# Performance work log

Measured on AMD Instinct MI355X. Metric: run time of the kernel, lower is better.

## Reference

```python
import jax, jax.numpy as jnp
import numpy as np

B, C, H, W = 32, 1024, 32, 32  # NOTE: code requires C == H*W (see bmm below)
C_HALF = C // 2


def setup_inputs() -> dict:
    key = jax.random.key(0)
    ks = jax.random.split(key, 7)
    s_in = 1.0 / np.sqrt(C)
    return {
        "x": jax.random.normal(ks[0], (B, C, H, W), dtype=jnp.float32),
        "Wq": jax.random.normal(ks[1], (C_HALF, C), dtype=jnp.float32) * s_in,
        "bq": jax.random.normal(ks[2], (C_HALF,), dtype=jnp.float32) * 0.01,
        "Wk": jax.random.normal(ks[3], (C_HALF, C), dtype=jnp.float32) * s_in,
        "bk": jax.random.normal(ks[4], (C_HALF,), dtype=jnp.float32) * 0.01,
        "Wv": jax.random.normal(ks[5], (C, C), dtype=jnp.float32) * s_in,
        "bv": jax.random.normal(ks[6], (C,), dtype=jnp.float32) * 0.01,
    }


def reference(x, Wq, bq, Wk, bk, Wv, bv):
    b, c, h, w = x.shape
    hw = h * w
    xf = x.reshape(b, c, hw)  # [B, C, HW]
    # 1x1 convs are per-pixel linear maps over channels
    q = jnp.einsum('oc,bcn->bno', Wq, xf) + bq            # [B, HW, C/2]  (permuted)
    k = jnp.einsum('oc,bcn->bon', Wk, xf) + bk[:, None]   # [B, C/2, HW]
    v = jnp.einsum('oc,bcn->bno', Wv, xf) + bv            # [B, HW, C]   (permuted)
    attn = jax.nn.softmax(jnp.einsum('bno,bom->bnm', q, k), axis=-1)  # [B, HW, HW]
    # torch: bmm(value [B,HW,C], attention^T [B,HW,HW]) -> requires C == HW
    out = jnp.einsum('bik,bjk->bij', v, attn)  # [B, HW(=C), HW]
    out = out.reshape(b, c, h, w)
    return out + x
```

## Files before the change

kernel.cpp:

```cpp
#include <hip/hip_runtime.h>

typedef _Float16 f16;
typedef _Float16 f16x8 __attribute__((ext_vector_type(8)));
typedef float f32x16 __attribute__((ext_vector_type(16)));

__device__ __forceinline__ void g2lds16(const void* g, void* l) {
    __builtin_amdgcn_global_load_lds(
        (const __attribute__((address_space(1))) void*)g,
        (__attribute__((address_space(3))) void*)l, 16, 0, 0);
}

__global__ __launch_bounds__(256)
void prep_w(const float* __restrict__ Wq, const float* __restrict__ bq,
            const float* __restrict__ Wk, const float* __restrict__ bk,
            const float* __restrict__ Wv, const float* __restrict__ bv,
            f16* __restrict__ Wall, float* __restrict__ ball)
{
    const int idx = blockIdx.x * 256 + threadIdx.x;
    const int o = idx >> 10;
    const int c = idx & 1023;
    float w;
    if (o < 512)        w = Wq[idx];
    else if (o < 1024)  w = Wk[idx - 512 * 1024];
    else                w = Wv[idx - 1024 * 1024];
    Wall[idx] = (f16)w;
    if (c == 0)
        ball[o] = (o < 512) ? bq[o] : (o < 1024) ? bk[o - 512] : bv[o - 1024];
}

__global__ __launch_bounds__(256)
void transpose_cast(const float* __restrict__ x, f16* __restrict__ xT)
{
    __shared__ float t[64][65];
    const int b  = blockIdx.z;
    const int c0 = blockIdx.y << 6;
    const int n0 = blockIdx.x << 6;
    const int tid = threadIdx.x;
    const float* xb = x + (unsigned long long)b * (1024ull * 1024ull);

    {
        const int cl = tid >> 4;
        const int n4 = (tid & 15) << 2;
#pragma unroll
        for (int i = 0; i < 64; i += 16) {
            const float4 v = *(const float4*)(xb + (unsigned long long)(c0 + cl + i) * 1024ull + (n0 + n4));
            t[cl + i][n4 + 0] = v.x; t[cl + i][n4 + 1] = v.y;
            t[cl + i][n4 + 2] = v.z; t[cl + i][n4 + 3] = v.w;
        }
    }
    __syncthreads();
    {
        f16* ob = xT + (unsigned long long)b * (1024ull * 1024ull);
        const int nl = tid >> 3;
        const int c8 = (tid & 7) << 3;
#pragma unroll
        for (int i = 0; i < 64; i += 32) {
            f16x8 h;
#pragma unroll
            for (int j = 0; j < 8; ++j) h[j] = (f16)t[c8 + j][nl + i];
            *(f16x8*)(ob + (unsigned long long)(n0 + nl + i) * 1024ull + (c0 + c8)) = h;
        }
    }
}

template <int EPI, int LDA, int LDB, int K, int LDO,
          long long SA, long long SB, long long SO, int SWZ>
__global__ __launch_bounds__(256, 4)
void gemm_nt(const f16* __restrict__ A, const f16* __restrict__ Bm,
             const float* __restrict__ bias,
             f16* __restrict__ Oh, float* __restrict__ Of,
             const float* __restrict__ Xres)
{
    __shared__ f16 As[128 * 64];
    __shared__ f16 Bs[128 * 64];

    const int tid  = threadIdx.x;
    const int wave = tid >> 6;
    const int lane = tid & 63;
    const int l31  = lane & 31;
    const int half = lane >> 5;
    const int wr   = (wave >> 1) << 6;
    const int wc   = (wave & 1) << 6;

    int bm, bn, bz = blockIdx.z;
    if (SWZ == 1) {
        const int xcd   = blockIdx.x & 7;
        const int local = blockIdx.x >> 3;
        const int stl   = local >> 5;
        const int sub   = local & 31;
        const int bng   = xcd & 1;
        const int g4    = stl * 4 + (xcd >> 1);
        bm = (g4 * 4 + (sub & 3)) << 7;
        bn = (bng * 8 + (sub >> 2)) << 7;
    } else if (SWZ == 2) {
        const int xcd   = blockIdx.x & 7;
        const int local = blockIdx.x >> 3;
        const int unit  = local >> 5;
        const int wi    = local & 31;
        const int pp    = unit * 8 + xcd;
        bz = pp >> 1;
        const int bh = pp & 1;
        bm = (wi & 7) << 7;
        bn = ((bh << 2) + (wi >> 3)) << 7;
    } else {
        bm = blockIdx.x << 7;
        bn = blockIdx.y << 7;
    }

    const f16* Ab = A  + (unsigned long long)bz * (unsigned long long)SA;
    const f16* Bb = Bm + (unsigned long long)bz * (unsigned long long)SB;

    const int srow = lane >> 3;
    const int scol = (((lane & 7) ^ srow) << 3);

    f32x16 acc[2][2] = {};

    for (int k0 = 0; k0 < K; k0 += 64) {
        __syncthreads();
#pragma unroll
        for (int t = 0; t < 4; ++t) {
            const int rb = t * 32 + wave * 8;
            g2lds16(Ab + (unsigned long long)(bm + rb + srow) * LDA + (k0 + scol),
                    As + rb * 64 + lane * 8);
            g2lds16(Bb + (unsigned long long)(bn + rb + srow) * LDB + (k0 + scol),
                    Bs + rb * 64 + lane * 8);
        }
        __syncthreads();

#pragma unroll
        for (int ks = 0; ks < 4; ++ks) {
            const int kg = ks * 2 + half;
            f16x8 af[2], bf[2];
#pragma unroll
            for (int i = 0; i < 2; ++i) {
                const int ra = wr + i * 32 + l31;
                af[i] = *(const f16x8*)(As + ra * 64 + ((kg ^ (ra & 7)) << 3));
                const int rbn = wc + i * 32 + l31;
                bf[i] = *(const f16x8*)(Bs + rbn * 64 + ((kg ^ (rbn & 7)) << 3));
            }
#pragma unroll
            for (int mi = 0; mi < 2; ++mi)
#pragma unroll
                for (int ni = 0; ni < 2; ++ni)
                    acc[mi][ni] = __builtin_amdgcn_mfma_f32_32x32x16_f16(
                        af[mi], bf[ni], acc[mi][ni], 0, 0, 0);
        }
    }

#pragma unroll
    for (int mi = 0; mi < 2; ++mi) {
#pragma unroll
        for (int ni = 0; ni < 2; ++ni) {
            const int col = bn + wc + ni * 32 + l31;
            float bc = 0.0f;
            if (EPI == 0) bc = bias[col];
#pragma unroll
            for (int r = 0; r < 16; ++r) {
                const int row = bm + wr + mi * 32 + (r & 3) + 8 * (r >> 2) + 4 * half;
                const float val = acc[mi][ni][r];
                if (EPI == 0) {
                    Oh[(unsigned long long)row * LDO + col] = (f16)(val + bc);
                } else if (EPI == 1) {
                    Of[(unsigned long long)bz * (unsigned long long)SO +
                       (unsigned long long)row * LDO + col] = val;
                } else {
                    const unsigned long long off =
                        (unsigned long long)bz * (unsigned long long)SO +
                        (unsigned long long)row * LDO + col;
                    Of[off] = val + Xres[off];
                }
            }
        }
    }
}

__global__ __launch_bounds__(512)
void qk_softmax(const f16* __restrict__ QKV, f16* __restrict__ P)
{
    __shared__ f16 Qs[32 * 512];
    __shared__ f16 Ks[512 * 64];
    __shared__ float redm[8][2][16];
    __shared__ float reds[8][2][16];

    const int tid  = threadIdx.x;
    const int wave = tid >> 6;
    const int lane = tid & 63;
    const int l31  = lane & 31;
    const int half = lane >> 5;

    const int xcd   = blockIdx.x & 7;
    const int local = blockIdx.x >> 3;
    const int batch = xcd * 4 + (local >> 5);
    const int jt    = local & 31;
    const int j0    = jt << 5;

    const f16* Qb = QKV + (unsigned long long)batch * (1024ull * 2048ull);
    const f16* Kb = Qb + 512;

#pragma unroll
    for (int i = 0; i < 4; ++i) {
        const int row = wave * 4 + i;
        g2lds16(Qb + (unsigned long long)(j0 + row) * 2048ull + ((lane ^ (row & 7)) << 3),
                Qs + row * 512 + lane * 8);
    }

    f32x16 acc[4] = {};
    const int wkey = wave << 7;

    for (int d0 = 0; d0 < 512; d0 += 32) {
        __syncthreads();
#pragma unroll
        for (int t = 0; t < 8; ++t) {
            const int rb  = wave * 64 + t * 8;
            const int R   = rb + (lane >> 3);
            const int p   = (lane & 7) ^ (R & 7);
            const int key = (R << 1) + (p >> 2);
            const int slt = p & 3;
            g2lds16(Kb + (unsigned long long)key * 2048ull + d0 + (slt << 3),
                    Ks + rb * 64 + lane * 8);
        }
        __syncthreads();
#pragma unroll
        for (int ks = 0; ks < 2; ++ks) {
            const int sl = ks * 2 + half;
            const int gs = (d0 >> 3) + sl;
            const f16x8 af = *(const f16x8*)(Qs + l31 * 512 + ((gs ^ (l31 & 7)) << 3));
#pragma unroll
            for (int ni = 0; ni < 4; ++ni) {
                const int key = wkey + ni * 32 + l31;
                const int R   = key >> 1;
                const int p   = ((key & 1) << 2) + sl;
                const f16x8 bf = *(const f16x8*)(Ks + R * 64 + ((p ^ (R & 7)) << 3));
                acc[ni] = __builtin_amdgcn_mfma_f32_32x32x16_f16(af, bf, acc[ni], 0, 0, 0);
            }
        }
    }

    float mx[16];
#pragma unroll
    for (int r = 0; r < 16; ++r) {
        float m = fmaxf(fmaxf(acc[0][r], acc[1][r]), fmaxf(acc[2][r], acc[3][r]));
#pragma unroll
        for (int off = 16; off; off >>= 1)
            m = fmaxf(m, __shfl_xor(m, off, 64));
        mx[r] = m;
    }
    if (l31 == 0) {
#pragma unroll
        for (int r = 0; r < 16; ++r) redm[wave][half][r] = mx[r];
    }
    __syncthreads();
#pragma unroll
    for (int r = 0; r < 16; ++r) {
        float m = redm[0][half][r];
#pragma unroll
        for (int w = 1; w < 8; ++w) m = fmaxf(m, redm[w][half][r]);
        mx[r] = m;
    }

    float sm[16];
#pragma unroll
    for (int r = 0; r < 16; ++r) sm[r] = 0.0f;
#pragma unroll
    for (int ni = 0; ni < 4; ++ni)
#pragma unroll
        for (int r = 0; r < 16; ++r) {
            const float e = __expf(acc[ni][r] - mx[r]);
            acc[ni][r] = e;
            sm[r] += e;
        }
#pragma unroll
    for (int r = 0; r < 16; ++r) {
#pragma unroll
        for (int off = 16; off; off >>= 1)
            sm[r] += __shfl_xor(sm[r], off, 64);
    }
    if (l31 == 0) {
#pragma unroll
        for (int r = 0; r < 16; ++r) reds[wave][half][r] = sm[r];
    }
    __syncthreads();
#pragma unroll
    for (int r = 0; r < 16; ++r) {
        float s = reds[0][half][r];
#pragma unroll
        for (int w = 1; w < 8; ++w) s += reds[w][half][r];
        sm[r] = 1.0f / s;
    }

    f16* Pt = Ks;
#pragma unroll
    for (int ni = 0; ni < 4; ++ni)
#pragma unroll
        for (int r = 0; r < 16; ++r) {
            const int row = (r & 3) + 8 * (r >> 2) + 4 * half;
            const int key = wkey + ni * 32 + l31;
            Pt[row * 1024 + key] = (f16)(acc[ni][r] * sm[r]);
        }
    __syncthreads();

    f16* Pg = P + ((unsigned long long)batch * 1024ull + j0) * 1024ull;
#pragma unroll
    for (int i = 0; i < 8; ++i)
        *(f16x8*)(Pg + i * 4096 + tid * 8) = *(const f16x8*)(Pt + i * 4096 + tid * 8);
}

extern "C" void kernel_launch(void* const* d_in, const int* in_sizes, int n_in,
                              void* d_out, int out_size, void* d_ws, size_t ws_size,
                              hipStream_t stream)
{
    const float* x  = (const float*)d_in[0];
    const float* Wq = (const float*)d_in[1];
    const float* bq = (const float*)d_in[2];
    const float* Wk = (const float*)d_in[3];
    const float* bk = (const float*)d_in[4];
    const float* Wv = (const float*)d_in[5];
    const float* bv = (const float*)d_in[6];
    float* out = (float*)d_out;

    f16*   xT   = (f16*)d_ws;
    f16*   Wall = xT + 32ull * 1024 * 1024;
    float* ball = (float*)(Wall + 2048ull * 1024);
    f16*   QKV  = (f16*)(ball + 2048);
    f16*   P    = QKV + 64ull * 1024 * 1024;

    prep_w<<<8192, 256, 0, stream>>>(Wq, bq, Wk, bk, Wv, bv, Wall, ball);
    transpose_cast<<<dim3(16, 16, 32), 256, 0, stream>>>(x, xT);

    gemm_nt<0, 1024, 1024, 1024, 2048, 0ll, 0ll, 0ll, 1>
        <<<dim3(4096, 1, 1), 256, 0, stream>>>(
        xT, Wall, ball, QKV, nullptr, nullptr);

    qk_softmax<<<dim3(1024, 1, 1), 512, 0, stream>>>(QKV, P);

    gemm_nt<2, 2048, 1024, 1024, 1024, 1024ll * 2048, 1024ll * 1024, 1024ll * 1024, 2>
        <<<dim3(2048, 1, 1), 256, 0, stream>>>(
        QKV + 1024, P, nullptr, nullptr, out, x);
}
```

Before: 650.4 us.

## Double query tile per block and double-buffer per-wave K loads in qk_softmax

The QK^T+softmax kernel now processes 64 query rows per block instead of 32, halving the grid and reusing each loaded K tile for twice as many rows. K loads become per-wave, double-buffered direct-to-LDS transfers gated by vmcnt waits instead of block-wide syncthreads, and MFMA sections get raised scheduling priority. This is meant to cut K reload traffic and barrier stalls, at the cost of more LDS (~96KB) and doubled accumulator registers, which may reduce occupancy. The softmax reductions and P write-out are done in two passes.

Measured after the change: 600.2 us. 1.08x faster.

```diff
diff --git a/kernel.cpp b/kernel.cpp
--- a/kernel.cpp
+++ b/kernel.cpp
@@ -177,10 +177,10 @@
 __global__ __launch_bounds__(512)
 void qk_softmax(const f16* __restrict__ QKV, f16* __restrict__ P)
 {
-    __shared__ f16 Qs[32 * 512];
-    __shared__ f16 Ks[512 * 64];
-    __shared__ float redm[8][2][16];
-    __shared__ float reds[8][2][16];
+    __shared__ f16 Qs[64 * 512];
+    __shared__ f16 Ks[2 * 8 * 2048];
+    __shared__ float redm[8][2][2][16];
+    __shared__ float reds[8][2][2][16];
 
     const int tid  = threadIdx.x;
     const int wave = tid >> 6;
@@ -190,119 +190,159 @@
 
     const int xcd   = blockIdx.x & 7;
     const int local = blockIdx.x >> 3;
-    const int batch = xcd * 4 + (local >> 5);
-    const int jt    = local & 31;
-    const int j0    = jt << 5;
+    const int batch = xcd * 4 + (local >> 4);
+    const int j0    = (local & 15) << 6;
 
     const f16* Qb = QKV + (unsigned long long)batch * (1024ull * 2048ull);
     const f16* Kb = Qb + 512;
 
 #pragma unroll
-    for (int i = 0; i < 4; ++i) {
-        const int row = wave * 4 + i;
-        g2lds16(Qb + (unsigned long long)(j0 + row) * 2048ull + ((lane ^ (row & 7)) << 3),
+    for (int i = 0; i < 8; ++i) {
+        const int row = wave * 8 + i;
+        g2lds16(Qb + (unsigned long long)(j0 + row) * 2048ull + ((lane ^ i) << 3),
                 Qs + row * 512 + lane * 8);
     }
-
-    f32x16 acc[4] = {};
-    const int wkey = wave << 7;
-
-    for (int d0 = 0; d0 < 512; d0 += 32) {
+    const int lu = lane ^ ((lane >> 3) & 1);
+    const f16* Kw = Kb + (unsigned long long)(wave * 128 + (lu >> 1)) * 2048ull
+                       + ((lu & 1) << 3);
+    f16* KsW = Ks + wave * 2048;
+#pragma unroll
+    for (int i = 0; i < 4; ++i)
+        g2lds16(Kw + i * (32 * 2048), KsW + i * 512 + lane * 8);
+
+    asm volatile("s_waitcnt vmcnt(0)" ::: "memory");
+    __builtin_amdgcn_sched_barrier(0);
+    __syncthreads();
+
+    const int r7 = l31 & 7;
+    const int sb = ((l31 << 1) + half) ^ ((l31 >> 2) & 1);
+    const f16* KsR = Ks + wave * 2048 + sb * 8;
+
+    f32x16 acc[2][4] = {};
+
+    for (int tt = 0; tt < 16; ++tt) {
+#pragma unroll
+        for (int p = 0; p < 2; ++p) {
+            const int t = tt * 2 + p;
+            if (t < 31) {
+#pragma unroll
+                for (int i = 0; i < 4; ++i)
+                    g2lds16(Kw + (t + 1) * 16 + i * (32 * 2048),
+                            KsW + (p ^ 1) * 16384 + i * 512 + lane * 8);
+                asm volatile("s_waitcnt vmcnt(4)" ::: "memory");
+            } else {
+                asm volatile("s_waitcnt vmcnt(0)" ::: "memory");
+            }
+            __builtin_amdgcn_sched_barrier(0);
+
+            const int gs = t * 2 + half;
+            f16x8 af[2];
+#pragma unroll
+            for (int sub = 0; sub < 2; ++sub)
+                af[sub] = *(const f16x8*)(Qs + (sub * 32 + l31) * 512 + ((gs ^ r7) << 3));
+            f16x8 bf[4];
+#pragma unroll
+            for (int ni = 0; ni < 4; ++ni)
+                bf[ni] = *(const f16x8*)(KsR + p * 16384 + ni * 512);
+
+            __builtin_amdgcn_s_setprio(1);
+#pragma unroll
+            for (int sub = 0; sub < 2; ++sub)
+#pragma unroll
+                for (int ni = 0; ni < 4; ++ni)
+                    acc[sub][ni] = __builtin_amdgcn_mfma_f32_32x32x16_f16(
+                        af[sub], bf[ni], acc[sub][ni], 0, 0, 0);
+            __builtin_amdgcn_s_setprio(0);
+        }
+    }
+
+    float mx[2][16];
+#pragma unroll
+    for (int sub = 0; sub < 2; ++sub)
+#pragma unroll
+        for (int r = 0; r < 16; ++r) {
+            float m = fmaxf(fmaxf(acc[sub][0][r], acc[sub][1][r]),
+                            fmaxf(acc[sub][2][r], acc[sub][3][r]));
+#pragma unroll
+            for (int off = 16; off; off >>= 1)
+                m = fmaxf(m, __shfl_xor(m, off, 64));
+            mx[sub][r] = m;
+        }
+    if (l31 == 0) {
+#pragma unroll
+        for (int sub = 0; sub < 2; ++sub)
+#pragma unroll
+            for (int r = 0; r < 16; ++r) redm[wave][sub][half][r] = mx[sub][r];
+    }
+    __syncthreads();
+#pragma unroll
+    for (int sub = 0; sub < 2; ++sub)
+#pragma unroll
+        for (int r = 0; r < 16; ++r) {
+            float m = redm[0][sub][half][r];
+#pragma unroll
+            for (int w = 1; w < 8; ++w) m = fmaxf(m, redm[w][sub][half][r]);
+            mx[sub][r] = m;
+        }
+
+    float sm[2][16];
+#pragma unroll
+    for (int sub = 0; sub < 2; ++sub)
+#pragma unroll
+        for (int r = 0; r < 16; ++r) sm[sub][r] = 0.0f;
+#pragma unroll
+    for (int sub = 0; sub < 2; ++sub)
+#pragma unroll
+        for (int ni = 0; ni < 4; ++ni)
+#pragma unroll
+            for (int r = 0; r < 16; ++r) {
+                const float e = __expf(acc[sub][ni][r] - mx[sub][r]);
+                acc[sub][ni][r] = e;
+                sm[sub][r] += e;
+            }
+#pragma unroll
+    for (int sub = 0; sub < 2; ++sub)
+#pragma unroll
+        for (int r = 0; r < 16; ++r) {
+#pragma unroll
+            for (int off = 16; off; off >>= 1)
+                sm[sub][r] += __shfl_xor(sm[sub][r], off, 64);
+        }
+    if (l31 == 0) {
+#pragma unroll
+        for (int sub = 0; sub < 2; ++sub)
+#pragma unroll
+            for (int r = 0; r < 16; ++r) reds[wave][sub][half][r] = sm[sub][r];
+    }
+    __syncthreads();
+#pragma unroll
+    for (int sub = 0; sub < 2; ++sub)
+#pragma unroll
+        for (int r = 0; r < 16; ++r) {
+            float s = reds[0][sub][half][r];
+#pragma unroll
+            for (int w = 1; w < 8; ++w) s += reds[w][sub][half][r];
+            sm[sub][r] = 1.0f / s;
+        }
+
+    f16* Pt = Ks;
+#pragma unroll
+    for (int pass = 0; pass < 2; ++pass) {
         __syncthreads();
 #pragma unroll
-        for (int t = 0; t < 8; ++t) {
-            const int rb  = wave * 64 + t * 8;
-            const int R   = rb + (lane >> 3);
-            const int p   = (lane & 7) ^ (R & 7);
-            const int key = (R << 1) + (p >> 2);
-            const int slt = p & 3;
-            g2lds16(Kb + (unsigned long long)key * 2048ull + d0 + (slt << 3),
-                    Ks + rb * 64 + lane * 8);
-        }
+        for (int ni = 0; ni < 4; ++ni)
+#pragma unroll
+            for (int r = 0; r < 16; ++r) {
+                const int row = (r & 3) + 8 * (r >> 2) + 4 * half;
+                const int key = (wave << 7) + ni * 32 + l31;
+                Pt[row * 1024 + key] = (f16)(acc[pass][ni][r] * sm[pass][r]);
+            }
         __syncthreads();
-#pragma unroll
-        for (int ks = 0; ks < 2; ++ks) {
-            const int sl = ks * 2 + half;
-            const int gs = (d0 >> 3) + sl;
-            const f16x8 af = *(const f16x8*)(Qs + l31 * 512 + ((gs ^ (l31 & 7)) << 3));
-#pragma unroll
-            for (int ni = 0; ni < 4; ++ni) {
-                const int key = wkey + ni * 32 + l31;
-                const int R   = key >> 1;
-                const int p   = ((key & 1) << 2) + sl;
-                const f16x8 bf = *(const f16x8*)(Ks + R * 64 + ((p ^ (R & 7)) << 3));
-                acc[ni] = __builtin_amdgcn_mfma_f32_32x32x16_f16(af, bf, acc[ni], 0, 0, 0);
-            }
-        }
-    }
-
-    float mx[16];
-#pragma unroll
-    for (int r = 0; r < 16; ++r) {
-        float m = fmaxf(fmaxf(acc[0][r], acc[1][r]), fmaxf(acc[2][r], acc[3][r]));
-#pragma unroll
-        for (int off = 16; off; off >>= 1)
-            m = fmaxf(m, __shfl_xor(m, off, 64));
-        mx[r] = m;
-    }
-    if (l31 == 0) {
-#pragma unroll
-        for (int r = 0; r < 16; ++r) redm[wave][half][r] = mx[r];
-    }
-    __syncthreads();
-#pragma unroll
-    for (int r = 0; r < 16; ++r) {
-        float m = redm[0][half][r];
-#pragma unroll
-        for (int w = 1; w < 8; ++w) m = fmaxf(m, redm[w][half][r]);
-        mx[r] = m;
-    }
-
-    float sm[16];
-#pragma unroll
-    for (int r = 0; r < 16; ++r) sm[r] = 0.0f;
-#pragma unroll
-    for (int ni = 0; ni < 4; ++ni)
-#pragma unroll
-        for (int r = 0; r < 16; ++r) {
-            const float e = __expf(acc[ni][r] - mx[r]);
-            acc[ni][r] = e;
-            sm[r] += e;
-        }
-#pragma unroll
-    for (int r = 0; r < 16; ++r) {
-#pragma unroll
-        for (int off = 16; off; off >>= 1)
-            sm[r] += __shfl_xor(sm[r], off, 64);
-    }
-    if (l31 == 0) {
-#pragma unroll
-        for (int r = 0; r < 16; ++r) reds[wave][half][r] = sm[r];
-    }
-    __syncthreads();
-#pragma unroll
-    for (int r = 0; r < 16; ++r) {
-        float s = reds[0][half][r];
-#pragma unroll
-        for (int w = 1; w < 8; ++w) s += reds[w][half][r];
-        sm[r] = 1.0f / s;
-    }
-
-    f16* Pt = Ks;
-#pragma unroll
-    for (int ni = 0; ni < 4; ++ni)
-#pragma unroll
-        for (int r = 0; r < 16; ++r) {
-            const int row = (r & 3) + 8 * (r >> 2) + 4 * half;
-            const int key = wkey + ni * 32 + l31;
-            Pt[row * 1024 + key] = (f16)(acc[ni][r] * sm[r]);
-        }
-    __syncthreads();
-
-    f16* Pg = P + ((unsigned long long)batch * 1024ull + j0) * 1024ull;
-#pragma unroll
-    for (int i = 0; i < 8; ++i)
-        *(f16x8*)(Pg + i * 4096 + tid * 8) = *(const f16x8*)(Pt + i * 4096 + tid * 8);
+        f16* Pg = P + ((unsigned long long)batch * 1024ull + j0 + pass * 32) * 1024ull;
+#pragma unroll
+        for (int i = 0; i < 8; ++i)
+            *(f16x8*)(Pg + i * 4096 + tid * 8) = *(const f16x8*)(Pt + i * 4096 + tid * 8);
+    }
 }
 
 extern "C" void kernel_launch(void* const* d_in, const int* in_sizes, int n_in,
@@ -331,7 +371,7 @@
         <<<dim3(4096, 1, 1), 256, 0, stream>>>(
         xT, Wall, ball, QKV, nullptr, nullptr);
 
-    qk_softmax<<<dim3(1024, 1, 1), 512, 0, stream>>>(QKV, P);
+    qk_softmax<<<dim3(512, 1, 1), 512, 0, stream>>>(QKV, P);
 
     gemm_nt<2, 2048, 1024, 1024, 1024, 1024ll * 2048, 1024ll * 1024, 1024ll * 1024, 2>
         <<<dim3(2048, 1, 1), 256, 0, stream>>>(
```

## Load Q/K fragments directly from global into registers in qk_softmax

Applied to the files above, without the earlier changes.

Replaces the LDS-staged Q and K tiles (global_load_lds plus two barriers per k-step) with direct per-lane global vector loads into MFMA operand registers, double-buffered two steps ahead. LDS is cut to just the P output staging buffer, and launch bounds now request 4 blocks per CU for higher occupancy. This removes the per-iteration barriers and LDS traffic. In exchange, each wave reads K rows straight from global/L2 with strided 16-byte accesses, with no sharing of Q across waves through LDS, which may raise cache traffic.

Measured after the change: 666.2 us. 1.02x slower.

```diff
diff --git a/kernel.cpp b/kernel.cpp
--- a/kernel.cpp
+++ b/kernel.cpp
@@ -174,11 +174,10 @@
     }
 }
 
-__global__ __launch_bounds__(512)
+__global__ __launch_bounds__(512, 4)
 void qk_softmax(const f16* __restrict__ QKV, f16* __restrict__ P)
 {
-    __shared__ f16 Qs[32 * 512];
-    __shared__ f16 Ks[512 * 64];
+    __shared__ f16 Pt[32 * 1024];
     __shared__ float redm[8][2][16];
     __shared__ float reds[8][2][16];
 
@@ -191,47 +190,44 @@
     const int xcd   = blockIdx.x & 7;
     const int local = blockIdx.x >> 3;
     const int batch = xcd * 4 + (local >> 5);
-    const int jt    = local & 31;
-    const int j0    = jt << 5;
+    const int j0    = (local & 31) << 5;
 
     const f16* Qb = QKV + (unsigned long long)batch * (1024ull * 2048ull);
     const f16* Kb = Qb + 512;
 
-#pragma unroll
-    for (int i = 0; i < 4; ++i) {
-        const int row = wave * 4 + i;
-        g2lds16(Qb + (unsigned long long)(j0 + row) * 2048ull + ((lane ^ (row & 7)) << 3),
-                Qs + row * 512 + lane * 8);
-    }
+    const f16* Qrow = Qb + (unsigned long long)(j0 + l31) * 2048ull + half * 8;
+    const f16* Kp0  = Kb + (unsigned long long)(wave * 128 + l31) * 2048ull + half * 8;
+    const f16* Kp1  = Kp0 + 32ull * 2048ull;
+    const f16* Kp2  = Kp0 + 64ull * 2048ull;
+    const f16* Kp3  = Kp0 + 96ull * 2048ull;
 
     f32x16 acc[4] = {};
-    const int wkey = wave << 7;
-
-    for (int d0 = 0; d0 < 512; d0 += 32) {
-        __syncthreads();
-#pragma unroll
-        for (int t = 0; t < 8; ++t) {
-            const int rb  = wave * 64 + t * 8;
-            const int R   = rb + (lane >> 3);
-            const int p   = (lane & 7) ^ (R & 7);
-            const int key = (R << 1) + (p >> 2);
-            const int slt = p & 3;
-            g2lds16(Kb + (unsigned long long)key * 2048ull + d0 + (slt << 3),
-                    Ks + rb * 64 + lane * 8);
-        }
-        __syncthreads();
-#pragma unroll
-        for (int ks = 0; ks < 2; ++ks) {
-            const int sl = ks * 2 + half;
-            const int gs = (d0 >> 3) + sl;
-            const f16x8 af = *(const f16x8*)(Qs + l31 * 512 + ((gs ^ (l31 & 7)) << 3));
-#pragma unroll
-            for (int ni = 0; ni < 4; ++ni) {
-                const int key = wkey + ni * 32 + l31;
-                const int R   = key >> 1;
-                const int p   = ((key & 1) << 2) + sl;
-                const f16x8 bf = *(const f16x8*)(Ks + R * 64 + ((p ^ (R & 7)) << 3));
-                acc[ni] = __builtin_amdgcn_mfma_f32_32x32x16_f16(af, bf, acc[ni], 0, 0, 0);
+    f16x8 qb_[2], kb0[2], kb1[2], kb2[2], kb3[2];
+
+#pragma unroll
+    for (int i = 0; i < 2; ++i) {
+        qb_[i] = *(const f16x8*)(Qrow + i * 16);
+        kb0[i] = *(const f16x8*)(Kp0 + i * 16);
+        kb1[i] = *(const f16x8*)(Kp1 + i * 16);
+        kb2[i] = *(const f16x8*)(Kp2 + i * 16);
+        kb3[i] = *(const f16x8*)(Kp3 + i * 16);
+    }
+
+    for (int tt = 0; tt < 16; ++tt) {
+#pragma unroll
+        for (int p = 0; p < 2; ++p) {
+            const int t = tt * 2 + p;
+            acc[0] = __builtin_amdgcn_mfma_f32_32x32x16_f16(qb_[p], kb0[p], acc[0], 0, 0, 0);
+            acc[1] = __builtin_amdgcn_mfma_f32_32x32x16_f16(qb_[p], kb1[p], acc[1], 0, 0, 0);
+            acc[2] = __builtin_amdgcn_mfma_f32_32x32x16_f16(qb_[p], kb2[p], acc[2], 0, 0, 0);
+            acc[3] = __builtin_amdgcn_mfma_f32_32x32x16_f16(qb_[p], kb3[p], acc[3], 0, 0, 0);
+            if (t + 2 < 32) {
+                const int off = (t + 2) * 16;
+                qb_[p] = *(const f16x8*)(Qrow + off);
+                kb0[p] = *(const f16x8*)(Kp0 + off);
+                kb1[p] = *(const f16x8*)(Kp1 + off);
+                kb2[p] = *(const f16x8*)(Kp2 + off);
+                kb3[p] = *(const f16x8*)(Kp3 + off);
             }
         }
     }
@@ -288,7 +284,7 @@
         sm[r] = 1.0f / s;
     }
 
-    f16* Pt = Ks;
+    const int wkey = wave << 7;
 #pragma unroll
     for (int ni = 0; ni < 4; ++ni)
 #pragma unroll
```
